# Performance work log

Measured on AMD Instinct MI355X. Metric: run time of the kernel, lower is better.

The kernel has to match this reference:

```python
import jax, jax.numpy as jnp
import numpy as np

# Normalizer hyperparameters (from init_kwargs)
THETA = 0.3     # final temperature theta
THETA0 = 4.0    # initial annealing temperature
T = 20          # number of annealing iterations
BETA = 0.7      # temperature decay
P = 0.1         # fraction -> k = p * (# finite entries per row)
TEMPERATURE = 1.0

BSZ, SEQ = 4096, 8192


def setup_inputs() -> dict:
    key = jax.random.key(0)
    k1, k2 = jax.random.split(key)
    score = jax.random.normal(k1, (BSZ, SEQ), dtype=jnp.float32)
    mask = jax.random.randint(k2, (BSZ, SEQ), 0, 2, dtype=jnp.int32)
    return {"score": score, "mask": mask}


def reference(score, mask):
    # score: [bsz, seq], mask: [bsz, seq] (0 = masked out)
    score = score * TEMPERATURE
    score = jnp.where(mask == 0, -jnp.inf, score)

    # k = p * number of finite (unmasked) entries per row
    k = jnp.sum(jnp.isfinite(score), axis=-1, keepdims=True).astype(score.dtype) * P

    # annealed temperature schedule: theta_t = max(beta^t * theta0, theta)
    thetas = [max(BETA ** t * THETA0, THETA) for t in range(T)]

    a = jnp.zeros((score.shape[0], 1), dtype=score.dtype)
    b = jnp.zeros_like(score)
    for th in thetas:
        # masked entries: exp(-inf)=0, relu(-inf)=0 -> they contribute nothing
        s = jnp.sum(jnp.exp((score + b) / th), axis=-1, keepdims=True)  # [bsz,1]
        a = th * jnp.log(k / (s + 1e-20))                               # [bsz,1]
        b = -jax.nn.relu(score + a)                                     # [bsz,seq]

    gamma = jnp.exp((score + a + b) / THETA)  # [bsz, seq]
    return gamma
```

## Files before the change

kernel.cpp:

```cpp
#include <hip/hip_runtime.h>
#include <math.h>

#define SEQ      8192
#define NTHREADS 256
#define VPT      32
#define F4PT     8

__device__ __forceinline__ float wave_sum(float x) {
    #pragma unroll
    for (int off = 32; off > 0; off >>= 1)
        x += __shfl_xor(x, off, 64);
    return x;
}

__global__ __launch_bounds__(NTHREADS) void normalizer_kernel(
        const float* __restrict__ score,
        const int*   __restrict__ mask,
        float*       __restrict__ out)
{
    const int row  = blockIdx.x;
    const int tid  = threadIdx.x;
    const int wid  = tid >> 6;
    const int lane = tid & 63;

    const float4* __restrict__ s4 = (const float4*)(score + (size_t)row * SEQ);
    const int4*   __restrict__ m4 = (const int4*)(mask  + (size_t)row * SEQ);

    float v[VPT];
    int cnt = 0;
    #pragma unroll
    for (int j = 0; j < F4PT; ++j) {
        float4 s = s4[j * NTHREADS + tid];
        int4   m = m4[j * NTHREADS + tid];
        v[4*j+0] = m.x ? s.x : -INFINITY;
        v[4*j+1] = m.y ? s.y : -INFINITY;
        v[4*j+2] = m.z ? s.z : -INFINITY;
        v[4*j+3] = m.w ? s.w : -INFINITY;
        cnt += (m.x != 0) + (m.y != 0) + (m.z != 0) + (m.w != 0);
    }

    __shared__ float red[21][4];

    float p = wave_sum((float)cnt);
    if (lane == 0) red[0][wid] = p;
    __syncthreads();
    const float k     = 0.1f * (red[0][0] + red[0][1] + red[0][2] + red[0][3]);
    const float log2k = __builtin_amdgcn_logf(k);

    constexpr double L2E = 1.4426950408889634;
    constexpr double LN2 = 0.6931471805599453;

    float  negA = INFINITY;
    double thd  = 4.0;
    #pragma unroll
    for (int t = 0; t < 8; ++t) {
        const float c    = (float)(L2E / thd);
        const float thl2 = (float)(thd * LN2);
        float part = 0.f;
        #pragma unroll
        for (int j = 0; j < VPT; ++j)
            part += __builtin_amdgcn_exp2f(fminf(v[j], negA) * c);
        part = wave_sum(part);
        if (lane == 0) red[1 + t][wid] = part;
        __syncthreads();
        const float s = red[1+t][0] + red[1+t][1] + red[1+t][2] + red[1+t][3];
        negA = thl2 * (__builtin_amdgcn_logf(s + 1e-20f) - log2k);
        thd *= 0.7;
    }

    const float cf = (float)(L2E / 0.3);
    #pragma unroll
    for (int j = 0; j < VPT; ++j) v[j] *= cf;
    float NA = negA * cf;

    #pragma unroll
    for (int t = 8; t < 20; ++t) {
        float part = 0.f;
        #pragma unroll
        for (int j = 0; j < VPT; ++j)
            part += __builtin_amdgcn_exp2f(fminf(v[j], NA));
        part = wave_sum(part);
        if (lane == 0) red[1 + t][wid] = part;
        __syncthreads();
        const float s = red[1+t][0] + red[1+t][1] + red[1+t][2] + red[1+t][3];
        NA = __builtin_amdgcn_logf(s + 1e-20f) - log2k;
    }

    float4* __restrict__ o4 = (float4*)(out + (size_t)row * SEQ);
    #pragma unroll
    for (int j = 0; j < F4PT; ++j) {
        float w0 = v[4*j+0], w1 = v[4*j+1], w2 = v[4*j+2], w3 = v[4*j+3];
        float4 g;
        g.x = (w0 == -INFINITY) ? 0.f : __builtin_amdgcn_exp2f(fminf(w0 - NA, 0.f));
        g.y = (w1 == -INFINITY) ? 0.f : __builtin_amdgcn_exp2f(fminf(w1 - NA, 0.f));
        g.z = (w2 == -INFINITY) ? 0.f : __builtin_amdgcn_exp2f(fminf(w2 - NA, 0.f));
        g.w = (w3 == -INFINITY) ? 0.f : __builtin_amdgcn_exp2f(fminf(w3 - NA, 0.f));
        o4[j * NTHREADS + tid] = g;
    }
}

extern "C" void kernel_launch(void* const* d_in, const int* in_sizes, int n_in,
                              void* d_out, int out_size, void* d_ws, size_t ws_size,
                              hipStream_t stream) {
    const float* score = (const float*)d_in[0];
    const int*   mask  = (const int*)d_in[1];
    float*       out   = (float*)d_out;
    const int rows = in_sizes[0] / SEQ;
    normalizer_kernel<<<rows, NTHREADS, 0, stream>>>(score, mask, out);
}
```

Before: 341.0 us.

## Process two rows per block and drop exp from constant-theta iterations

Each block now handles two rows, sharing one barrier per iteration between both row reductions and giving more independent work between barriers. For the final twelve iterations, where theta is fixed at its floor, the scores are exponentiated once and each iteration's exp/log pair becomes a min against a scalar, so the per-element work is a min and an add. The output is computed as min(exp(w), e^NA) / e^NA instead of a fresh exp. This roughly doubles register use per thread and can overflow float range when exp2 of large scaled scores is precomputed; it also assumes an even number of rows.

```diff
diff --git a/kernel.cpp b/kernel.cpp
--- a/kernel.cpp
+++ b/kernel.cpp
@@ -5,6 +5,7 @@
 #define NTHREADS 256
 #define VPT      32
 #define F4PT     8
+#define RPB      2
 
 __device__ __forceinline__ float wave_sum(float x) {
     #pragma unroll
@@ -18,84 +19,127 @@
         const int*   __restrict__ mask,
         float*       __restrict__ out)
 {
-    const int row  = blockIdx.x;
+    const int row0 = blockIdx.x * RPB;
     const int tid  = threadIdx.x;
     const int wid  = tid >> 6;
     const int lane = tid & 63;
 
-    const float4* __restrict__ s4 = (const float4*)(score + (size_t)row * SEQ);
-    const int4*   __restrict__ m4 = (const int4*)(mask  + (size_t)row * SEQ);
+    constexpr double L2E = 1.4426950408889634;
+    const float cf = (float)(L2E / 0.3);
 
-    float v[VPT];
-    int cnt = 0;
+    const float4* __restrict__ sA = (const float4*)(score + (size_t)row0 * SEQ);
+    const int4*   __restrict__ mA = (const int4*)(mask  + (size_t)row0 * SEQ);
+    const float4* __restrict__ sB = (const float4*)(score + (size_t)(row0 + 1) * SEQ);
+    const int4*   __restrict__ mB = (const int4*)(mask  + (size_t)(row0 + 1) * SEQ);
+
+    float wA[VPT], wB[VPT];
+    int cntA = 0, cntB = 0;
     #pragma unroll
     for (int j = 0; j < F4PT; ++j) {
-        float4 s = s4[j * NTHREADS + tid];
-        int4   m = m4[j * NTHREADS + tid];
-        v[4*j+0] = m.x ? s.x : -INFINITY;
-        v[4*j+1] = m.y ? s.y : -INFINITY;
-        v[4*j+2] = m.z ? s.z : -INFINITY;
-        v[4*j+3] = m.w ? s.w : -INFINITY;
-        cnt += (m.x != 0) + (m.y != 0) + (m.z != 0) + (m.w != 0);
+        float4 s = sA[j * NTHREADS + tid];
+        int4   m = mA[j * NTHREADS + tid];
+        wA[4*j+0] = m.x ? s.x * cf : -INFINITY;
+        wA[4*j+1] = m.y ? s.y * cf : -INFINITY;
+        wA[4*j+2] = m.z ? s.z * cf : -INFINITY;
+        wA[4*j+3] = m.w ? s.w * cf : -INFINITY;
+        cntA += (m.x != 0) + (m.y != 0) + (m.z != 0) + (m.w != 0);
+    }
+    #pragma unroll
+    for (int j = 0; j < F4PT; ++j) {
+        float4 s = sB[j * NTHREADS + tid];
+        int4   m = mB[j * NTHREADS + tid];
+        wB[4*j+0] = m.x ? s.x * cf : -INFINITY;
+        wB[4*j+1] = m.y ? s.y * cf : -INFINITY;
+        wB[4*j+2] = m.z ? s.z * cf : -INFINITY;
+        wB[4*j+3] = m.w ? s.w * cf : -INFINITY;
+        cntB += (m.x != 0) + (m.y != 0) + (m.z != 0) + (m.w != 0);
     }
 
-    __shared__ float red[21][4];
+    __shared__ float red[21][RPB][4];
 
-    float p = wave_sum((float)cnt);
-    if (lane == 0) red[0][wid] = p;
+    float pA = wave_sum((float)cntA);
+    float pB = wave_sum((float)cntB);
+    if (lane == 0) { red[0][0][wid] = pA; red[0][1][wid] = pB; }
     __syncthreads();
-    const float k     = 0.1f * (red[0][0] + red[0][1] + red[0][2] + red[0][3]);
-    const float log2k = __builtin_amdgcn_logf(k);
+    const float kA = 0.1f * (red[0][0][0] + red[0][0][1] + red[0][0][2] + red[0][0][3]);
+    const float kB = 0.1f * (red[0][1][0] + red[0][1][1] + red[0][1][2] + red[0][1][3]);
+    const float l2kA = __builtin_amdgcn_logf(kA);
+    const float l2kB = __builtin_amdgcn_logf(kB);
+    const float rkA  = 1.0f / kA;
+    const float rkB  = 1.0f / kB;
 
-    constexpr double L2E = 1.4426950408889634;
-    constexpr double LN2 = 0.6931471805599453;
+    float NAa = INFINITY, NAb = INFINITY;
 
-    float  negA = INFINITY;
-    double thd  = 4.0;
+    double thd = 4.0;
     #pragma unroll
     for (int t = 0; t < 8; ++t) {
-        const float c    = (float)(L2E / thd);
-        const float thl2 = (float)(thd * LN2);
-        float part = 0.f;
+        const float cp  = (float)(0.3 / thd);
+        const float inv = (float)(thd / 0.3);
+        float a0 = 0.f, a1 = 0.f, b0 = 0.f, b1 = 0.f;
         #pragma unroll
-        for (int j = 0; j < VPT; ++j)
-            part += __builtin_amdgcn_exp2f(fminf(v[j], negA) * c);
-        part = wave_sum(part);
-        if (lane == 0) red[1 + t][wid] = part;
+        for (int j = 0; j < VPT; j += 2) {
+            a0 += __builtin_amdgcn_exp2f(fminf(wA[j],   NAa) * cp);
+            a1 += __builtin_amdgcn_exp2f(fminf(wA[j+1], NAa) * cp);
+            b0 += __builtin_amdgcn_exp2f(fminf(wB[j],   NAb) * cp);
+            b1 += __builtin_amdgcn_exp2f(fminf(wB[j+1], NAb) * cp);
+        }
+        float pa = wave_sum(a0 + a1);
+        float pb = wave_sum(b0 + b1);
+        if (lane == 0) { red[1+t][0][wid] = pa; red[1+t][1][wid] = pb; }
         __syncthreads();
-        const float s = red[1+t][0] + red[1+t][1] + red[1+t][2] + red[1+t][3];
-        negA = thl2 * (__builtin_amdgcn_logf(s + 1e-20f) - log2k);
+        const float sA_ = red[1+t][0][0] + red[1+t][0][1] + red[1+t][0][2] + red[1+t][0][3];
+        const float sB_ = red[1+t][1][0] + red[1+t][1][1] + red[1+t][1][2] + red[1+t][1][3];
+        NAa = inv * (__builtin_amdgcn_logf(sA_ + 1e-20f) - l2kA);
+        NAb = inv * (__builtin_amdgcn_logf(sB_ + 1e-20f) - l2kB);
         thd *= 0.7;
     }
 
-    const float cf = (float)(L2E / 0.3);
     #pragma unroll
-    for (int j = 0; j < VPT; ++j) v[j] *= cf;
-    float NA = negA * cf;
+    for (int j = 0; j < VPT; ++j) {
+        wA[j] = __builtin_amdgcn_exp2f(wA[j]);
+        wB[j] = __builtin_amdgcn_exp2f(wB[j]);
+    }
+    float eNAa = __builtin_amdgcn_exp2f(NAa);
+    float eNAb = __builtin_amdgcn_exp2f(NAb);
 
     #pragma unroll
     for (int t = 8; t < 20; ++t) {
-        float part = 0.f;
+        float a0 = 0.f, a1 = 0.f, b0 = 0.f, b1 = 0.f;
         #pragma unroll
-        for (int j = 0; j < VPT; ++j)
-            part += __builtin_amdgcn_exp2f(fminf(v[j], NA));
-        part = wave_sum(part);
-        if (lane == 0) red[1 + t][wid] = part;
+        for (int j = 0; j < VPT; j += 2) {
+            a0 += fminf(wA[j],   eNAa);
+            a1 += fminf(wA[j+1], eNAa);
+            b0 += fminf(wB[j],   eNAb);
+            b1 += fminf(wB[j+1], eNAb);
+        }
+        float pa = wave_sum(a0 + a1);
+        float pb = wave_sum(b0 + b1);
+        if (lane == 0) { red[1+t][0][wid] = pa; red[1+t][1][wid] = pb; }
         __syncthreads();
-        const float s = red[1+t][0] + red[1+t][1] + red[1+t][2] + red[1+t][3];
-        NA = __builtin_amdgcn_logf(s + 1e-20f) - log2k;
+        const float sA_ = red[1+t][0][0] + red[1+t][0][1] + red[1+t][0][2] + red[1+t][0][3];
+        const float sB_ = red[1+t][1][0] + red[1+t][1][1] + red[1+t][1][2] + red[1+t][1][3];
+        eNAa = (sA_ + 1e-20f) * rkA;
+        eNAb = (sB_ + 1e-20f) * rkB;
     }
 
-    float4* __restrict__ o4 = (float4*)(out + (size_t)row * SEQ);
+    const float ra = 1.0f / eNAa;
+    const float rb = 1.0f / eNAb;
+    float4* __restrict__ oA = (float4*)(out + (size_t)row0 * SEQ);
+    float4* __restrict__ oB = (float4*)(out + (size_t)(row0 + 1) * SEQ);
     #pragma unroll
     for (int j = 0; j < F4PT; ++j) {
-        float w0 = v[4*j+0], w1 = v[4*j+1], w2 = v[4*j+2], w3 = v[4*j+3];
         float4 g;
-        g.x = (w0 == -INFINITY) ? 0.f : __builtin_amdgcn_exp2f(fminf(w0 - NA, 0.f));
-        g.y = (w1 == -INFINITY) ? 0.f : __builtin_amdgcn_exp2f(fminf(w1 - NA, 0.f));
-        g.z = (w2 == -INFINITY) ? 0.f : __builtin_amdgcn_exp2f(fminf(w2 - NA, 0.f));
-        g.w = (w3 == -INFINITY) ? 0.f : __builtin_amdgcn_exp2f(fminf(w3 - NA, 0.f));
-        o4[j * NTHREADS + tid] = g;
+        g.x = fminf(wA[4*j+0], eNAa) * ra;
+        g.y = fminf(wA[4*j+1], eNAa) * ra;
+        g.z = fminf(wA[4*j+2], eNAa) * ra;
+        g.w = fminf(wA[4*j+3], eNAa) * ra;
+        oA[j * NTHREADS + tid] = g;
+        float4 h;
+        h.x = fminf(wB[4*j+0], eNAb) * rb;
+        h.y = fminf(wB[4*j+1], eNAb) * rb;
+        h.z = fminf(wB[4*j+2], eNAb) * rb;
+        h.w = fminf(wB[4*j+3], eNAb) * rb;
+        oB[j * NTHREADS + tid] = h;
     }
 }
 
@@ -106,5 +150,5 @@
     const int*   mask  = (const int*)d_in[1];
     float*       out   = (float*)d_out;
     const int rows = in_sizes[0] / SEQ;
-    normalizer_kernel<<<rows, NTHREADS, 0, stream>>>(score, mask, out);
+    normalizer_kernel<<<rows / RPB, NTHREADS, 0, stream>>>(score, mask, out);
 }
```

Measured after the change: 336.7 us. Within noise of the previous version (-1.3%).

## Map one row per wave and move final-temperature iterations to linear domain

Applied to the files above, without the earlier changes.

Each wavefront now processes a whole row with 128 values per lane, which removes the shared-memory reductions and block barriers. For the 12 iterations at the fixed final temperature, values are exponentiated once, and each iteration becomes min plus sum in linear space with no per-element exp2. The output is formed by a multiply instead of exp2. This raises register pressure to 128 floats per lane and cuts the number of waves available to hide memory latency, and there are overflow and precision risks from working in the exponentiated domain.

```diff
diff --git a/kernel.cpp b/kernel.cpp
--- a/kernel.cpp
+++ b/kernel.cpp
@@ -3,8 +3,9 @@
 
 #define SEQ      8192
 #define NTHREADS 256
-#define VPT      32
-#define F4PT     8
+#define WPB      4
+#define VPT      128
+#define F4PT     32
 
 __device__ __forceinline__ float wave_sum(float x) {
     #pragma unroll
@@ -13,89 +14,86 @@
     return x;
 }
 
-__global__ __launch_bounds__(NTHREADS) void normalizer_kernel(
+__global__ __launch_bounds__(NTHREADS, 2) void normalizer_kernel(
         const float* __restrict__ score,
         const int*   __restrict__ mask,
         float*       __restrict__ out)
 {
-    const int row  = blockIdx.x;
     const int tid  = threadIdx.x;
     const int wid  = tid >> 6;
     const int lane = tid & 63;
+    const int row  = blockIdx.x * WPB + wid;
+
+    constexpr double L2E = 1.4426950408889634;
+    const float cf = (float)(L2E / 0.3);
 
     const float4* __restrict__ s4 = (const float4*)(score + (size_t)row * SEQ);
     const int4*   __restrict__ m4 = (const int4*)(mask  + (size_t)row * SEQ);
 
-    float v[VPT];
-    int cnt = 0;
+    float w[VPT];
+    float cntf = 0.f;
     #pragma unroll
     for (int j = 0; j < F4PT; ++j) {
-        float4 s = s4[j * NTHREADS + tid];
-        int4   m = m4[j * NTHREADS + tid];
-        v[4*j+0] = m.x ? s.x : -INFINITY;
-        v[4*j+1] = m.y ? s.y : -INFINITY;
-        v[4*j+2] = m.z ? s.z : -INFINITY;
-        v[4*j+3] = m.w ? s.w : -INFINITY;
-        cnt += (m.x != 0) + (m.y != 0) + (m.z != 0) + (m.w != 0);
+        float4 s = s4[j * 64 + lane];
+        int4   m = m4[j * 64 + lane];
+        w[4*j+0] = m.x ? s.x * cf : -INFINITY;
+        w[4*j+1] = m.y ? s.y * cf : -INFINITY;
+        w[4*j+2] = m.z ? s.z * cf : -INFINITY;
+        w[4*j+3] = m.w ? s.w * cf : -INFINITY;
+        cntf += (float)((m.x != 0) + (m.y != 0) + (m.z != 0) + (m.w != 0));
     }
 
-    __shared__ float red[21][4];
+    const float k    = 0.1f * wave_sum(cntf);
+    const float l2k  = __builtin_amdgcn_logf(k);
+    const float rk   = 1.0f / k;
 
-    float p = wave_sum((float)cnt);
-    if (lane == 0) red[0][wid] = p;
-    __syncthreads();
-    const float k     = 0.1f * (red[0][0] + red[0][1] + red[0][2] + red[0][3]);
-    const float log2k = __builtin_amdgcn_logf(k);
+    float NA  = INFINITY;
+    float cp  = 0.075f;
+    float inv = 13.333333f;
 
-    constexpr double L2E = 1.4426950408889634;
-    constexpr double LN2 = 0.6931471805599453;
-
-    float  negA = INFINITY;
-    double thd  = 4.0;
-    #pragma unroll
     for (int t = 0; t < 8; ++t) {
-        const float c    = (float)(L2E / thd);
-        const float thl2 = (float)(thd * LN2);
-        float part = 0.f;
+        float a0 = 0.f, a1 = 0.f, a2 = 0.f, a3 = 0.f;
         #pragma unroll
-        for (int j = 0; j < VPT; ++j)
-            part += __builtin_amdgcn_exp2f(fminf(v[j], negA) * c);
-        part = wave_sum(part);
-        if (lane == 0) red[1 + t][wid] = part;
-        __syncthreads();
-        const float s = red[1+t][0] + red[1+t][1] + red[1+t][2] + red[1+t][3];
-        negA = thl2 * (__builtin_amdgcn_logf(s + 1e-20f) - log2k);
-        thd *= 0.7;
+        for (int j = 0; j < VPT; j += 4) {
+            a0 += __builtin_amdgcn_exp2f(fminf(w[j+0], NA) * cp);
+            a1 += __builtin_amdgcn_exp2f(fminf(w[j+1], NA) * cp);
+            a2 += __builtin_amdgcn_exp2f(fminf(w[j+2], NA) * cp);
+            a3 += __builtin_amdgcn_exp2f(fminf(w[j+3], NA) * cp);
+        }
+        const float s = wave_sum((a0 + a1) + (a2 + a3));
+        NA = inv * (__builtin_amdgcn_logf(s + 1e-20f) - l2k);
+        cp  *= 1.4285715f;
+        inv *= 0.7f;
     }
 
-    const float cf = (float)(L2E / 0.3);
     #pragma unroll
-    for (int j = 0; j < VPT; ++j) v[j] *= cf;
-    float NA = negA * cf;
+    for (int j = 0; j < VPT; ++j)
+        w[j] = __builtin_amdgcn_exp2f(w[j]);
+    float eNA = __builtin_amdgcn_exp2f(NA);
 
-    #pragma unroll
     for (int t = 8; t < 20; ++t) {
-        float part = 0.f;
+        float a0 = 0.f, a1 = 0.f, a2 = 0.f, a3 = 0.f;
         #pragma unroll
-        for (int j = 0; j < VPT; ++j)
-            part += __builtin_amdgcn_exp2f(fminf(v[j], NA));
-        part = wave_sum(part);
-        if (lane == 0) red[1 + t][wid] = part;
-        __syncthreads();
-        const float s = red[1+t][0] + red[1+t][1] + red[1+t][2] + red[1+t][3];
-        NA = __builtin_amdgcn_logf(s + 1e-20f) - log2k;
+        for (int j = 0; j < VPT; j += 4) {
+            a0 += fminf(w[j+0], eNA);
+            a1 += fminf(w[j+1], eNA);
+            a2 += fminf(w[j+2], eNA);
+            a3 += fminf(w[j+3], eNA);
+        }
+        const float s = wave_sum((a0 + a1) + (a2 + a3));
+        eNA = (s + 1e-20f) * rk;
     }
 
+    const float r = 1.0f / eNA;
     float4* __restrict__ o4 = (float4*)(out + (size_t)row * SEQ);
     #pragma unroll
     for (int j = 0; j < F4PT; ++j) {
-        float w0 = v[4*j+0], w1 = v[4*j+1], w2 = v[4*j+2], w3 = v[4*j+3];
         float4 g;
-        g.x = (w0 == -INFINITY) ? 0.f : __builtin_amdgcn_exp2f(fminf(w0 - NA, 0.f));
-        g.y = (w1 == -INFINITY) ? 0.f : __builtin_amdgcn_exp2f(fminf(w1 - NA, 0.f));
-        g.z = (w2 == -INFINITY) ? 0.f : __builtin_amdgcn_exp2f(fminf(w2 - NA, 0.f));
-        g.w = (w3 == -INFINITY) ? 0.f : __builtin_amdgcn_exp2f(fminf(w3 - NA, 0.f));
-        o4[j * NTHREADS + tid] = g;
+        g.x = fminf(w[4*j+0], eNA) * r;
+        g.y = fminf(w[4*j+1], eNA) * r;
+        g.z = fminf(w[4*j+2], eNA) * r;
+        g.w = fminf(w[4*j+3], eNA) * r;
+        o4[j * 64 + lane] = g;
     }
 }
 
@@ -106,5 +104,5 @@
     const int*   mask  = (const int*)d_in[1];
     float*       out   = (float*)d_out;
     const int rows = in_sizes[0] / SEQ;
-    normalizer_kernel<<<rows, NTHREADS, 0, stream>>>(score, mask, out);
+    normalizer_kernel<<<rows / WPB, NTHREADS, 0, stream>>>(score, mask, out);
 }
```

Result: slower. 453.0 us (+32.8%).
